# Performance work log

Measured on AMD Instinct MI355X. Metric: run time of the kernel, lower is better.

## Reference

```python
import jax, jax.numpy as jnp
import numpy as np

B, S, D = 4, 2048, 1024


def setup_inputs() -> dict:
    key = jax.random.key(0)
    ks = jax.random.split(key, 7)
    s = 1.0 / np.sqrt(D)
    return {
        "x": jax.random.normal(ks[0], (B, S, D), dtype=jnp.float32),
        "Wq": jax.random.normal(ks[1], (D, D), dtype=jnp.float32) * s,
        "bq": jnp.zeros((D,), dtype=jnp.float32),
        "Wk": jax.random.normal(ks[2], (D, D), dtype=jnp.float32) * s,
        "bk": jnp.zeros((D,), dtype=jnp.float32),
        "Wv": jax.random.normal(ks[3], (D, D), dtype=jnp.float32) * s,
        "bv": jnp.zeros((D,), dtype=jnp.float32),
    }


def reference(x, Wq, bq, Wk, bk, Wv, bv):
    # Linear layers: x @ W^T + b (torch nn.Linear convention)
    Q = jnp.einsum("bsd,ed->bse", x, Wq) + bq
    K = jnp.einsum("bsd,ed->bse", x, Wk) + bk
    V = jnp.einsum("bsd,ed->bse", x, Wv) + bv
    scale = 1.0 / (x.shape[-1] ** 0.5)
    scores = jnp.einsum("bse,bte->bst", Q, K) * scale  # [B, S, S]
    attn = jax.nn.softmax(scores, axis=-1)
    out = jnp.einsum("bst,bte->bse", attn, V)
    return out
```

## Files before the change

### kernel.cpp

```cpp
#include <hip/hip_runtime.h>
#include <math.h>


typedef _Float16 f16;
typedef _Float16 f16x8 __attribute__((ext_vector_type(8)));
typedef _Float16 f16x4 __attribute__((ext_vector_type(4)));
typedef float f32x4 __attribute__((ext_vector_type(4)));

__device__ __forceinline__ void glds16(const void* g, const void* l) {
    __builtin_amdgcn_global_load_lds(
        (const __attribute__((address_space(1))) void*)g,
        (__attribute__((address_space(3))) void*)l, 16, 0, 0);
}

#define VMCNT(n)  asm volatile("s_waitcnt vmcnt(" #n ")" ::: "memory")
#define LGKM(n)   asm volatile("s_waitcnt lgkmcnt(" #n ")" ::: "memory")
#define BARRIER() asm volatile("s_barrier" ::: "memory")
#define SCHEDB()  __builtin_amdgcn_sched_barrier(0)

__global__ __launch_bounds__(256) void cvt16_kernel(
    const float* __restrict__ in, f16* __restrict__ o, int n4)
{
    int i = blockIdx.x * 256 + threadIdx.x;
    if (i >= n4) return;
    float4 v = ((const float4*)in)[i];
    f16x4 h = { (f16)v.x, (f16)v.y, (f16)v.z, (f16)v.w };
    ((f16x4*)o)[i] = h;
}

__global__ __launch_bounds__(256) void cvtw_kernel(
    const float* __restrict__ Wq, const float* __restrict__ Wk,
    const float* __restrict__ Wv, f16* __restrict__ o, int n4)
{
    int i = blockIdx.x * 256 + threadIdx.x;
    if (i >= n4) return;
    const float* src = (blockIdx.y == 0) ? Wq : (blockIdx.y == 1) ? Wk : Wv;
    float4 v = ((const float4*)src)[i];
    f16x4 h = { (f16)v.x, (f16)v.y, (f16)v.z, (f16)v.w };
    ((f16x4*)(o + (size_t)blockIdx.y * 1024 * 1024))[i] = h;
}

__global__ __launch_bounds__(256) void zero_kernel(float* __restrict__ p, int n)
{
    int i = blockIdx.x * 256 + threadIdx.x;
    if (i < n) p[i] = 0.0f;
}

#define ABUF 16384
#define BBUF 8192
#define BOFF 49152

__device__ __forceinline__ void frag_read16(
    const f16* __restrict__ sA, const f16* __restrict__ sB,
    int wr, int wc, int lr, int kq, f16x8 a[2][4], f16x8 b[2][4])
{
    #pragma unroll
    for (int kk = 0; kk < 2; ++kk) {
        const int c = kk * 4 + kq;
        #pragma unroll
        for (int i = 0; i < 4; ++i) {
            const int ar = wr * 64 + i * 16 + lr;
            a[kk][i] = *(const f16x8*)&sA[ar * 64 + ((c ^ (ar & 7)) * 8)];
        }
        #pragma unroll
        for (int j = 0; j < 4; ++j) {
            const int br = wc * 64 + j * 16 + lr;
            b[kk][j] = *(const f16x8*)&sB[br * 64 + ((c ^ (br & 7)) * 8)];
        }
    }
}

__device__ __forceinline__ void mfma32(
    const f16x8 a[2][4], const f16x8 b[2][4], f32x4 acc[4][4])
{
    #pragma unroll
    for (int kk = 0; kk < 2; ++kk)
        #pragma unroll
        for (int i = 0; i < 4; ++i)
            #pragma unroll
            for (int j = 0; j < 4; ++j)
                acc[i][j] = __builtin_amdgcn_mfma_f32_16x16x32_f16(a[kk][i], b[kk][j], acc[i][j], 0, 0, 0);
}

__device__ __forceinline__ void mfma_core3(
    const f16* __restrict__ A, int lda,
    const f16* __restrict__ B, int ldb,
    int K, int m0, int n0, f16* sm, f32x4 acc[4][4])
{
    const int tid  = threadIdx.x;
    const int lane = tid & 63;
    const int w    = tid >> 6;
    const int wr   = w >> 1;
    const int wc   = w & 1;
    const int lr   = lane & 15;
    const int kq   = lane >> 4;

    const int rl = lane >> 3;
    const int ch = (lane & 7) ^ rl;

    const f16* gA[4];
    #pragma unroll
    for (int p = 0; p < 4; ++p)
        gA[p] = A + (size_t)(m0 + p * 64 + w * 8 + rl) * lda + ch * 8;
    const f16* gB[2];
    #pragma unroll
    for (int p = 0; p < 2; ++p)
        gB[p] = B + (size_t)(n0 + p * 64 + w * 8 + rl) * ldb + ch * 8;

    const int NT = K >> 6;

    f16* sA0 = sm;             f16* sB0 = sm + BOFF;
    f16* sA1 = sm + ABUF;      f16* sB1 = sm + BOFF + BBUF;
    f16* sA2 = sm + 2 * ABUF;  f16* sB2 = sm + BOFF + 2 * BBUF;

    #define STAGE(kofs, dA, dB) do {                                          \
        _Pragma("unroll")                                                     \
        for (int p = 0; p < 4; ++p)                                           \
            glds16(gA[p] + (kofs), (dA) + w * 512 + p * 4096);                \
        _Pragma("unroll")                                                     \
        for (int p = 0; p < 2; ++p)                                           \
            glds16(gB[p] + (kofs), (dB) + w * 512 + p * 4096);                \
    } while (0)

    STAGE(0,  sA0, sB0);
    STAGE(64, sA1, sB1);
    VMCNT(6);
    BARRIER();
    f16x8 a0[2][4], b0[2][4], a1[2][4], b1[2][4];
    frag_read16(sA0, sB0, wr, wc, lr, kq, a0, b0);

    for (int t = 0; t < NT; t += 2) {
        if (t + 2 < NT) { STAGE((t + 2) * 64, sA2, sB2); VMCNT(6); }
        else            { VMCNT(0); }
        BARRIER();
        frag_read16(sA1, sB1, wr, wc, lr, kq, a1, b1);
        LGKM(15);
        SCHEDB();
        __builtin_amdgcn_s_setprio(1);
        mfma32(a0, b0, acc);
        __builtin_amdgcn_s_setprio(0);
        BARRIER();

        if (t + 3 < NT) { STAGE((t + 3) * 64, sA0, sB0); }
        if (t + 2 < NT) {
            if (t + 3 < NT) { VMCNT(6); } else { VMCNT(0); }
        }
        BARRIER();
        if (t + 2 < NT) {
            frag_read16(sA2, sB2, wr, wc, lr, kq, a0, b0);
            LGKM(15);
        } else {
            LGKM(0);
        }
        SCHEDB();
        __builtin_amdgcn_s_setprio(1);
        mfma32(a1, b1, acc);
        __builtin_amdgcn_s_setprio(0);
        BARRIER();

        f16* tA = sA2; sA2 = sA1; sA1 = sA0; sA0 = tA;
        f16* tB = sB2; sB2 = sB1; sB1 = sB0; sB0 = tB;
    }
    #undef STAGE
}

__global__ __launch_bounds__(512, 2) void qkv_mfma_kernel(
    const f16* __restrict__ xh, const f16* __restrict__ Wh,
    const float* __restrict__ bq, const float* __restrict__ bk,
    const float* __restrict__ bv,
    f16* __restrict__ Qh, f16* __restrict__ Kh, f16* __restrict__ Vh)
{
    extern __shared__ __align__(16) f16 smem[];
    int flat = blockIdx.x + 8 * (blockIdx.y + 32 * blockIdx.z);
    flat = (flat & 7) * 96 + (flat >> 3);
    const int bx = flat & 7;
    const int by = (flat >> 3) & 31;
    const int bz = flat >> 8;

    const int m0 = by * 256;
    const int n0 = bx * 128;

    f32x4 acc[4][4];
    #pragma unroll
    for (int i = 0; i < 4; ++i)
        #pragma unroll
        for (int j = 0; j < 4; ++j) acc[i][j] = (f32x4){0.f, 0.f, 0.f, 0.f};

    mfma_core3(xh, 1024, Wh + (size_t)bz * 1024 * 1024, 1024, 1024, m0, n0, smem, acc);

    const float* bias = (bz == 0) ? bq : (bz == 1) ? bk : bv;
    const float  sc   = (bz == 0) ? 0.03125f : 1.0f;
    f16* C = (bz == 0) ? Qh : (bz == 1) ? Kh : Vh;
    const int lane = threadIdx.x & 63;
    const int w    = threadIdx.x >> 6;
    const int wr = w >> 1, wc = w & 1;
    const int col  = lane & 15;
    const int quad = lane >> 4;

    #pragma unroll
    for (int j = 0; j < 4; ++j) {
        const int gn = n0 + wc * 64 + j * 16 + col;
        const float bb = bias[gn];
        #pragma unroll
        for (int i = 0; i < 4; ++i)
            #pragma unroll
            for (int r = 0; r < 4; ++r) {
                const int gm = m0 + wr * 64 + i * 16 + quad * 4 + r;
                C[(size_t)gm * 1024 + gn] = (f16)((acc[i][j][r] + bb) * sc);
            }
    }
}

__global__ __launch_bounds__(256) void vtrans_kernel(
    const f16* __restrict__ V, f16* __restrict__ Vt)
{
    __shared__ f16 t[64][72];
    const int b  = blockIdx.z;
    const int s0 = blockIdx.x * 64;
    const int d0 = blockIdx.y * 64;
    const int tid = threadIdx.x;

    const int r  = tid >> 3;
    const int c8 = (tid & 7) * 8;
    const f16* src = V + ((size_t)b * 2048 + s0) * 1024 + d0;
    *(f16x8*)&t[r][c8]      = *(const f16x8*)(src + (size_t)r * 1024 + c8);
    *(f16x8*)&t[r + 32][c8] = *(const f16x8*)(src + (size_t)(r + 32) * 1024 + c8);
    __syncthreads();

    const int dl  = tid >> 2;
    const int sl0 = (tid & 3) * 16;
    f16* dst = Vt + ((size_t)b * 1024 + d0 + dl) * 2048 + s0 + sl0;
    f16 buf[16];
    #pragma unroll
    for (int u = 0; u < 16; ++u) buf[u] = t[sl0 + u][dl];
    *(f16x8*)dst       = *(f16x8*)&buf[0];
    *(f16x8*)(dst + 8) = *(f16x8*)&buf[8];
}

__global__ __launch_bounds__(512, 2) void scores_exp_kernel(
    const f16* __restrict__ Qh, const f16* __restrict__ Kh,
    f16* __restrict__ P, float* __restrict__ sums)
{
    extern __shared__ __align__(16) f16 smem[];
    int flat = blockIdx.x + 16 * (blockIdx.y + 8 * blockIdx.z);
    flat = (flat & 7) * 64 + (flat >> 3);
    const int bx = flat & 15;
    const int by = (flat >> 4) & 7;
    const int b  = flat >> 7;

    const int m0 = by * 256;
    const int n0 = bx * 128;

    f32x4 acc[4][4];
    #pragma unroll
    for (int i = 0; i < 4; ++i)
        #pragma unroll
        for (int j = 0; j < 4; ++j) acc[i][j] = (f32x4){0.f, 0.f, 0.f, 0.f};

    const size_t ao = (size_t)b * 2048 * 1024;
    mfma_core3(Qh + ao, 1024, Kh + ao, 1024, 1024, m0, n0, smem, acc);

    const int lane = threadIdx.x & 63;
    const int w    = threadIdx.x >> 6;
    const int wr = w >> 1, wc = w & 1;
    const int col  = lane & 15;
    const int quad = lane >> 4;
    f16* C = P + (size_t)b * 2048 * 2048;

    float rp[4][4];
    #pragma unroll
    for (int i = 0; i < 4; ++i)
        #pragma unroll
        for (int r = 0; r < 4; ++r) rp[i][r] = 0.0f;

    #pragma unroll
    for (int i = 0; i < 4; ++i)
        #pragma unroll
        for (int r = 0; r < 4; ++r) {
            const int gm = m0 + wr * 64 + i * 16 + quad * 4 + r;
            #pragma unroll
            for (int j = 0; j < 4; ++j) {
                const int gn = n0 + wc * 64 + j * 16 + col;
                const f16 p = (f16)__expf(acc[i][j][r]);
                C[(size_t)gm * 2048 + gn] = p;
                rp[i][r] += (float)p;
            }
        }

    #pragma unroll
    for (int i = 0; i < 4; ++i)
        #pragma unroll
        for (int r = 0; r < 4; ++r) {
            float v = rp[i][r];
            v += __shfl_xor(v, 1);
            v += __shfl_xor(v, 2);
            v += __shfl_xor(v, 4);
            v += __shfl_xor(v, 8);
            rp[i][r] = v;
        }
    if (col == 0) {
        #pragma unroll
        for (int i = 0; i < 4; ++i)
            #pragma unroll
            for (int r = 0; r < 4; ++r) {
                const int row = m0 + wr * 64 + i * 16 + quad * 4 + r;
                atomicAdd(&sums[b * 2048 + row], rp[i][r]);
            }
    }
}

__global__ __launch_bounds__(512, 2) void pv_mfma_kernel(
    const f16* __restrict__ P, const f16* __restrict__ Vt,
    const float* __restrict__ sums, float* __restrict__ out)
{
    extern __shared__ __align__(16) f16 smem[];
    int flat = blockIdx.x + 8 * (blockIdx.y + 8 * blockIdx.z);
    flat = (flat & 7) * 32 + (flat >> 3);
    const int bx = flat & 7;
    const int by = (flat >> 3) & 7;
    const int b  = flat >> 6;

    const int m0 = by * 256;
    const int n0 = bx * 128;

    f32x4 acc[4][4];
    #pragma unroll
    for (int i = 0; i < 4; ++i)
        #pragma unroll
        for (int j = 0; j < 4; ++j) acc[i][j] = (f32x4){0.f, 0.f, 0.f, 0.f};

    const size_t ao = (size_t)b * 2048 * 2048;
    const size_t bo = (size_t)b * 1024 * 2048;
    mfma_core3(P + ao, 2048, Vt + bo, 2048, 2048, m0, n0, smem, acc);

    const int lane = threadIdx.x & 63;
    const int w    = threadIdx.x >> 6;
    const int wr = w >> 1, wc = w & 1;
    const int col  = lane & 15;
    const int quad = lane >> 4;
    float* C = out + (size_t)b * 2048 * 1024;

    #pragma unroll
    for (int i = 0; i < 4; ++i)
        #pragma unroll
        for (int r = 0; r < 4; ++r) {
            const int rowg = m0 + wr * 64 + i * 16 + quad * 4 + r;
            const float inv = 1.0f / sums[b * 2048 + rowg];
            #pragma unroll
            for (int j = 0; j < 4; ++j) {
                const int gn = n0 + wc * 64 + j * 16 + col;
                C[(size_t)rowg * 1024 + gn] = acc[i][j][r] * inv;
            }
        }
}

extern "C" void kernel_launch(void* const* d_in, const int* in_sizes, int n_in,
                              void* d_out, int out_size, void* d_ws, size_t ws_size,
                              hipStream_t stream)
{
    (void)in_sizes; (void)n_in; (void)out_size; (void)ws_size;
    const int Bn = 4, S = 2048, D = 1024;
    const float* x  = (const float*)d_in[0];
    const float* Wq = (const float*)d_in[1];
    const float* bq = (const float*)d_in[2];
    const float* Wk = (const float*)d_in[3];
    const float* bk = (const float*)d_in[4];
    const float* Wv = (const float*)d_in[5];
    const float* bv = (const float*)d_in[6];
    float* out = (float*)d_out;

    const size_t MB = 1024 * 1024;
    char* w = (char*)d_ws;
    f16*   xh   = (f16*)(w + 0 * MB);
    f16*   Wh3  = (f16*)(w + 16 * MB);
    f16*   Vh   = (f16*)(w + 22 * MB);
    f16*   Qh   = (f16*)(w + 38 * MB);
    f16*   Kh   = (f16*)(w + 54 * MB);
    f16*   Vt   = (f16*)(w + 70 * MB);
    float* sums = (float*)(w + 86 * MB);
    f16*   P    = (f16*)(w + 0 * MB);

    static bool attr_set = false;
    if (!attr_set) {
        (void)hipFuncSetAttribute(reinterpret_cast<const void*>(qkv_mfma_kernel),
                            hipFuncAttributeMaxDynamicSharedMemorySize, 147456);
        (void)hipFuncSetAttribute(reinterpret_cast<const void*>(scores_exp_kernel),
                            hipFuncAttributeMaxDynamicSharedMemorySize, 147456);
        (void)hipFuncSetAttribute(reinterpret_cast<const void*>(pv_mfma_kernel),
                            hipFuncAttributeMaxDynamicSharedMemorySize, 147456);
        attr_set = true;
    }

    cvt16_kernel<<<dim3(Bn * S * D / 4 / 256), 256, 0, stream>>>(x, xh, Bn * S * D / 4);
    cvtw_kernel<<<dim3(D * D / 4 / 256, 3), 256, 0, stream>>>(Wq, Wk, Wv, Wh3, D * D / 4);
    zero_kernel<<<dim3((Bn * S + 255) / 256), 256, 0, stream>>>(sums, Bn * S);

    qkv_mfma_kernel<<<dim3(D / 128, (Bn * S) / 256, 3), 512, 147456, stream>>>(
        xh, Wh3, bq, bk, bv, Qh, Kh, Vh);
    vtrans_kernel<<<dim3(S / 64, D / 64, Bn), 256, 0, stream>>>(Vh, Vt);

    scores_exp_kernel<<<dim3(S / 128, S / 256, Bn), 512, 147456, stream>>>(
        Qh, Kh, P, sums);
    pv_mfma_kernel<<<dim3(D / 128, S / 256, Bn), 512, 147456, stream>>>(
        P, Vt, sums, out);
}
```

Baseline: 267.9 us.

## Switch GEMMs to 256x256 tiles with double-buffered interleaved staging core

New measurement: 266.7 us. About the same (-0.4%).

```diff
diff --git a/kernel.cpp b/kernel.cpp
--- a/kernel.cpp
+++ b/kernel.cpp
@@ -46,122 +46,121 @@
     if (i < n) p[i] = 0.0f;
 }
 
-#define ABUF 16384
-#define BBUF 8192
-#define BOFF 49152
-
-__device__ __forceinline__ void frag_read16(
-    const f16* __restrict__ sA, const f16* __restrict__ sB,
-    int wr, int wc, int lr, int kq, f16x8 a[2][4], f16x8 b[2][4])
-{
-    #pragma unroll
-    for (int kk = 0; kk < 2; ++kk) {
-        const int c = kk * 4 + kq;
-        #pragma unroll
-        for (int i = 0; i < 4; ++i) {
-            const int ar = wr * 64 + i * 16 + lr;
-            a[kk][i] = *(const f16x8*)&sA[ar * 64 + ((c ^ (ar & 7)) * 8)];
-        }
-        #pragma unroll
-        for (int j = 0; j < 4; ++j) {
-            const int br = wc * 64 + j * 16 + lr;
-            b[kk][j] = *(const f16x8*)&sB[br * 64 + ((c ^ (br & 7)) * 8)];
-        }
-    }
-}
-
-__device__ __forceinline__ void mfma32(
-    const f16x8 a[2][4], const f16x8 b[2][4], f32x4 acc[4][4])
-{
-    #pragma unroll
-    for (int kk = 0; kk < 2; ++kk)
-        #pragma unroll
-        for (int i = 0; i < 4; ++i)
-            #pragma unroll
-            for (int j = 0; j < 4; ++j)
-                acc[i][j] = __builtin_amdgcn_mfma_f32_16x16x32_f16(a[kk][i], b[kk][j], acc[i][j], 0, 0, 0);
-}
-
-__device__ __forceinline__ void mfma_core3(
+__device__ __forceinline__ void core8(
     const f16* __restrict__ A, int lda,
     const f16* __restrict__ B, int ldb,
-    int K, int m0, int n0, f16* sm, f32x4 acc[4][4])
+    int K, int m0, int n0, f16* sm, f32x4 (&acc)[8][4])
 {
     const int tid  = threadIdx.x;
     const int lane = tid & 63;
     const int w    = tid >> 6;
-    const int wr   = w >> 1;
-    const int wc   = w & 1;
+    const int wr   = w >> 2;
+    const int wn   = w & 3;
     const int lr   = lane & 15;
     const int kq   = lane >> 4;
 
-    const int rl = lane >> 3;
-    const int ch = (lane & 7) ^ rl;
-
-    const f16* gA[4];
-    #pragma unroll
-    for (int p = 0; p < 4; ++p)
-        gA[p] = A + (size_t)(m0 + p * 64 + w * 8 + rl) * lda + ch * 8;
-    const f16* gB[2];
-    #pragma unroll
-    for (int p = 0; p < 2; ++p)
-        gB[p] = B + (size_t)(n0 + p * 64 + w * 8 + rl) * ldb + ch * 8;
-
-    const int NT = K >> 6;
-
-    f16* sA0 = sm;             f16* sB0 = sm + BOFF;
-    f16* sA1 = sm + ABUF;      f16* sB1 = sm + BOFF + BBUF;
-    f16* sA2 = sm + 2 * ABUF;  f16* sB2 = sm + BOFF + 2 * BBUF;
-
-    #define STAGE(kofs, dA, dB) do {                                          \
+    const int rl   = lane >> 3;
+    const int swz  = ((lane & 7) ^ rl) * 8;
+
+    const f16* baseA = A + (size_t)(m0 + w * 16 + rl) * lda + swz;
+    const f16* baseB = B + (size_t)(n0 + w * 16 + rl) * ldb + swz;
+
+    f16* curA = sm;             f16* curB = sm + 16384;
+    f16* othA = sm + 32768;     f16* othB = sm + 49152;
+
+    const int NT   = K >> 6;
+    const int wofs = w * 1024;
+
+    #define STG_A(dst, h, tt) do {                                            \
+        glds16(baseA + (size_t)((h) * 128 + 0) * lda + (size_t)(tt) * 64,     \
+               (dst) + (h) * 8192 + wofs);                                    \
+        glds16(baseA + (size_t)((h) * 128 + 8) * lda + (size_t)(tt) * 64,     \
+               (dst) + (h) * 8192 + wofs + 512);                              \
+    } while (0)
+    #define STG_B(dst, h, tt) do {                                            \
+        glds16(baseB + (size_t)((h) * 128 + 0) * ldb + (size_t)(tt) * 64,     \
+               (dst) + (h) * 8192 + wofs);                                    \
+        glds16(baseB + (size_t)((h) * 128 + 8) * ldb + (size_t)(tt) * 64,     \
+               (dst) + (h) * 8192 + wofs + 512);                              \
+    } while (0)
+    #define RD_A(dst4, mh, kk) do {                                           \
         _Pragma("unroll")                                                     \
-        for (int p = 0; p < 4; ++p)                                           \
-            glds16(gA[p] + (kofs), (dA) + w * 512 + p * 4096);                \
+        for (int i = 0; i < 4; ++i) {                                         \
+            const int ar = wr * 128 + (mh) * 64 + i * 16 + lr;                \
+            dst4[i] = *(const f16x8*)&curA[ar * 64 +                          \
+                        (((((kk) * 4 + kq)) ^ (ar & 7)) * 8)];                \
+        } } while (0)
+    #define RD_B(dst4, kk) do {                                               \
         _Pragma("unroll")                                                     \
-        for (int p = 0; p < 2; ++p)                                           \
-            glds16(gB[p] + (kofs), (dB) + w * 512 + p * 4096);                \
+        for (int j = 0; j < 4; ++j) {                                         \
+            const int br = wn * 64 + j * 16 + lr;                             \
+            dst4[j] = *(const f16x8*)&curB[br * 64 +                          \
+                        (((((kk) * 4 + kq)) ^ (br & 7)) * 8)];                \
+        } } while (0)
+    #define MFMA16(mh, av, bv) do {                                           \
+        _Pragma("unroll")                                                     \
+        for (int i = 0; i < 4; ++i)                                           \
+            _Pragma("unroll")                                                 \
+            for (int j = 0; j < 4; ++j)                                       \
+                acc[(mh) * 4 + i][j] = __builtin_amdgcn_mfma_f32_16x16x32_f16(\
+                    av[i], bv[j], acc[(mh) * 4 + i][j], 0, 0, 0);             \
     } while (0)
 
-    STAGE(0,  sA0, sB0);
-    STAGE(64, sA1, sB1);
-    VMCNT(6);
+    STG_B(curB, 0, 0); STG_B(curB, 1, 0);
+    STG_A(curA, 0, 0); STG_A(curA, 1, 0);
+    STG_B(othB, 0, 1); STG_B(othB, 1, 1);
+    VMCNT(4);
     BARRIER();
-    f16x8 a0[2][4], b0[2][4], a1[2][4], b1[2][4];
-    frag_read16(sA0, sB0, wr, wc, lr, kq, a0, b0);
-
-    for (int t = 0; t < NT; t += 2) {
-        if (t + 2 < NT) { STAGE((t + 2) * 64, sA2, sB2); VMCNT(6); }
-        else            { VMCNT(0); }
-        BARRIER();
-        frag_read16(sA1, sB1, wr, wc, lr, kq, a1, b1);
-        LGKM(15);
-        SCHEDB();
+
+    f16x8 a0[4], a1[4], b0[4], b1[4];
+
+    for (int t = 0; t < NT; ++t) {
+        const bool s1 = (t + 1 < NT);
+        const bool s2 = (t + 2 < NT);
+
+        RD_A(a0, 0, 0); RD_B(b0, 0);
+        if (s1) STG_A(othA, 0, t + 1);
+        BARRIER(); LGKM(0); SCHEDB();
         __builtin_amdgcn_s_setprio(1);
-        mfma32(a0, b0, acc);
+        MFMA16(0, a0, b0);
         __builtin_amdgcn_s_setprio(0);
         BARRIER();
 
-        if (t + 3 < NT) { STAGE((t + 3) * 64, sA0, sB0); }
-        if (t + 2 < NT) {
-            if (t + 3 < NT) { VMCNT(6); } else { VMCNT(0); }
-        }
-        BARRIER();
-        if (t + 2 < NT) {
-            frag_read16(sA2, sB2, wr, wc, lr, kq, a0, b0);
-            LGKM(15);
-        } else {
-            LGKM(0);
-        }
-        SCHEDB();
+        RD_A(a1, 0, 1); RD_B(b1, 1);
+        if (s1) STG_A(othA, 1, t + 1);
+        BARRIER(); LGKM(0); SCHEDB();
         __builtin_amdgcn_s_setprio(1);
-        mfma32(a1, b1, acc);
+        MFMA16(0, a1, b1);
         __builtin_amdgcn_s_setprio(0);
         BARRIER();
 
-        f16* tA = sA2; sA2 = sA1; sA1 = sA0; sA0 = tA;
-        f16* tB = sB2; sB2 = sB1; sB1 = sB0; sB0 = tB;
+        RD_A(a0, 1, 0);
+        if (s2) STG_B(curB, 0, t + 2);
+        BARRIER(); LGKM(0); SCHEDB();
+        __builtin_amdgcn_s_setprio(1);
+        MFMA16(1, a0, b0);
+        __builtin_amdgcn_s_setprio(0);
+        BARRIER();
+
+        RD_A(a1, 1, 1);
+        if (s2) STG_B(curB, 1, t + 2);
+        if (s2)      { VMCNT(4); }
+        else if (s1) { VMCNT(0); }
+        BARRIER(); LGKM(0); SCHEDB();
+        __builtin_amdgcn_s_setprio(1);
+        MFMA16(1, a1, b1);
+        __builtin_amdgcn_s_setprio(0);
+        BARRIER();
+
+        f16* x;
+        x = curA; curA = othA; othA = x;
+        x = curB; curB = othB; othB = x;
     }
-    #undef STAGE
+    #undef STG_A
+    #undef STG_B
+    #undef RD_A
+    #undef RD_B
+    #undef MFMA16
 }
 
 __global__ __launch_bounds__(512, 2) void qkv_mfma_kernel(
@@ -171,41 +170,41 @@
     f16* __restrict__ Qh, f16* __restrict__ Kh, f16* __restrict__ Vh)
 {
     extern __shared__ __align__(16) f16 smem[];
-    int flat = blockIdx.x + 8 * (blockIdx.y + 32 * blockIdx.z);
-    flat = (flat & 7) * 96 + (flat >> 3);
-    const int bx = flat & 7;
-    const int by = (flat >> 3) & 31;
-    const int bz = flat >> 8;
+    int flat = blockIdx.x + 4 * (blockIdx.y + 32 * blockIdx.z);
+    flat = (flat & 7) * 48 + (flat >> 3);
+    const int bx = flat & 3;
+    const int by = (flat >> 2) & 31;
+    const int bz = flat >> 7;
 
     const int m0 = by * 256;
-    const int n0 = bx * 128;
-
-    f32x4 acc[4][4];
-    #pragma unroll
-    for (int i = 0; i < 4; ++i)
+    const int n0 = bx * 256;
+
+    f32x4 acc[8][4];
+    #pragma unroll
+    for (int i = 0; i < 8; ++i)
         #pragma unroll
         for (int j = 0; j < 4; ++j) acc[i][j] = (f32x4){0.f, 0.f, 0.f, 0.f};
 
-    mfma_core3(xh, 1024, Wh + (size_t)bz * 1024 * 1024, 1024, 1024, m0, n0, smem, acc);
+    core8(xh, 1024, Wh + (size_t)bz * 1024 * 1024, 1024, 1024, m0, n0, smem, acc);
 
     const float* bias = (bz == 0) ? bq : (bz == 1) ? bk : bv;
     const float  sc   = (bz == 0) ? 0.03125f : 1.0f;
     f16* C = (bz == 0) ? Qh : (bz == 1) ? Kh : Vh;
     const int lane = threadIdx.x & 63;
     const int w    = threadIdx.x >> 6;
-    const int wr = w >> 1, wc = w & 1;
+    const int wr = w >> 2, wn = w & 3;
     const int col  = lane & 15;
     const int quad = lane >> 4;
 
     #pragma unroll
     for (int j = 0; j < 4; ++j) {
-        const int gn = n0 + wc * 64 + j * 16 + col;
+        const int gn = n0 + wn * 64 + j * 16 + col;
         const float bb = bias[gn];
         #pragma unroll
-        for (int i = 0; i < 4; ++i)
+        for (int i = 0; i < 8; ++i)
             #pragma unroll
             for (int r = 0; r < 4; ++r) {
-                const int gm = m0 + wr * 64 + i * 16 + quad * 4 + r;
+                const int gm = m0 + wr * 128 + i * 16 + quad * 4 + r;
                 C[(size_t)gm * 1024 + gn] = (f16)((acc[i][j][r] + bb) * sc);
             }
     }
@@ -242,45 +241,45 @@
     f16* __restrict__ P, float* __restrict__ sums)
 {
     extern __shared__ __align__(16) f16 smem[];
-    int flat = blockIdx.x + 16 * (blockIdx.y + 8 * blockIdx.z);
-    flat = (flat & 7) * 64 + (flat >> 3);
-    const int bx = flat & 15;
-    const int by = (flat >> 4) & 7;
-    const int b  = flat >> 7;
+    int flat = blockIdx.x + 8 * (blockIdx.y + 8 * blockIdx.z);
+    flat = (flat & 7) * 32 + (flat >> 3);
+    const int bx = flat & 7;
+    const int by = (flat >> 3) & 7;
+    const int b  = flat >> 6;
 
     const int m0 = by * 256;
-    const int n0 = bx * 128;
-
-    f32x4 acc[4][4];
-    #pragma unroll
-    for (int i = 0; i < 4; ++i)
+    const int n0 = bx * 256;
+
+    f32x4 acc[8][4];
+    #pragma unroll
+    for (int i = 0; i < 8; ++i)
         #pragma unroll
         for (int j = 0; j < 4; ++j) acc[i][j] = (f32x4){0.f, 0.f, 0.f, 0.f};
 
     const size_t ao = (size_t)b * 2048 * 1024;
-    mfma_core3(Qh + ao, 1024, Kh + ao, 1024, 1024, m0, n0, smem, acc);
+    core8(Qh + ao, 1024, Kh + ao, 1024, 1024, m0, n0, smem, acc);
 
     const int lane = threadIdx.x & 63;
     const int w    = threadIdx.x >> 6;
-    const int wr = w >> 1, wc = w & 1;
+    const int wr = w >> 2, wn = w & 3;
     const int col  = lane & 15;
     const int quad = lane >> 4;
     f16* C = P + (size_t)b * 2048 * 2048;
 
-    float rp[4][4];
-    #pragma unroll
-    for (int i = 0; i < 4; ++i)
+    float rp[8][4];
+    #pragma unroll
+    for (int i = 0; i < 8; ++i)
         #pragma unroll
         for (int r = 0; r < 4; ++r) rp[i][r] = 0.0f;
 
     #pragma unroll
-    for (int i = 0; i < 4; ++i)
+    for (int i = 0; i < 8; ++i)
         #pragma unroll
         for (int r = 0; r < 4; ++r) {
-            const int gm = m0 + wr * 64 + i * 16 + quad * 4 + r;
+            const int gm = m0 + wr * 128 + i * 16 + quad * 4 + r;
             #pragma unroll
             for (int j = 0; j < 4; ++j) {
-                const int gn = n0 + wc * 64 + j * 16 + col;
+                const int gn = n0 + wn * 64 + j * 16 + col;
                 const f16 p = (f16)__expf(acc[i][j][r]);
                 C[(size_t)gm * 2048 + gn] = p;
                 rp[i][r] += (float)p;
@@ -288,7 +287,7 @@
         }
 
     #pragma unroll
-    for (int i = 0; i < 4; ++i)
+    for (int i = 0; i < 8; ++i)
         #pragma unroll
         for (int r = 0; r < 4; ++r) {
             float v = rp[i][r];
@@ -300,10 +299,10 @@
         }
     if (col == 0) {
         #pragma unroll
-        for (int i = 0; i < 4; ++i)
+        for (int i = 0; i < 8; ++i)
             #pragma unroll
             for (int r = 0; r < 4; ++r) {
-                const int row = m0 + wr * 64 + i * 16 + quad * 4 + r;
+                const int row = m0 + wr * 128 + i * 16 + quad * 4 + r;
                 atomicAdd(&sums[b * 2048 + row], rp[i][r]);
             }
     }
@@ -314,41 +313,41 @@
     const float* __restrict__ sums, float* __restrict__ out)
 {
     extern __shared__ __align__(16) f16 smem[];
-    int flat = blockIdx.x + 8 * (blockIdx.y + 8 * blockIdx.z);
-    flat = (flat & 7) * 32 + (flat >> 3);
-    const int bx = flat & 7;
-    const int by = (flat >> 3) & 7;
-    const int b  = flat >> 6;
+    int flat = blockIdx.x + 4 * (blockIdx.y + 8 * blockIdx.z);
+    flat = (flat & 7) * 16 + (flat >> 3);
+    const int bx = flat & 3;
+    const int by = (flat >> 2) & 7;
+    const int b  = flat >> 5;
 
     const int m0 = by * 256;
-    const int n0 = bx * 128;
-
-    f32x4 acc[4][4];
-    #pragma unroll
-    for (int i = 0; i < 4; ++i)
+    const int n0 = bx * 256;
+
+    f32x4 acc[8][4];
+    #pragma unroll
+    for (int i = 0; i < 8; ++i)
         #pragma unroll
         for (int j = 0; j < 4; ++j) acc[i][j] = (f32x4){0.f, 0.f, 0.f, 0.f};
 
     const size_t ao = (size_t)b * 2048 * 2048;
     const size_t bo = (size_t)b * 1024 * 2048;
-    mfma_core3(P + ao, 2048, Vt + bo, 2048, 2048, m0, n0, smem, acc);
+    core8(P + ao, 2048, Vt + bo, 2048, 2048, m0, n0, smem, acc);
 
     const int lane = threadIdx.x & 63;
     const int w    = threadIdx.x >> 6;
-    const int wr = w >> 1, wc = w & 1;
+    const int wr = w >> 2, wn = w & 3;
     const int col  = lane & 15;
     const int quad = lane >> 4;
     float* C = out + (size_t)b * 2048 * 1024;
 
     #pragma unroll
-    for (int i = 0; i < 4; ++i)
+    for (int i = 0; i < 8; ++i)
         #pragma unroll
         for (int r = 0; r < 4; ++r) {
-            const int rowg = m0 + wr * 64 + i * 16 + quad * 4 + r;
+            const int rowg = m0 + wr * 128 + i * 16 + quad * 4 + r;
             const float inv = 1.0f / sums[b * 2048 + rowg];
             #pragma unroll
             for (int j = 0; j < 4; ++j) {
-                const int gn = n0 + wc * 64 + j * 16 + col;
+                const int gn = n0 + wn * 64 + j * 16 + col;
                 C[(size_t)rowg * 1024 + gn] = acc[i][j][r] * inv;
             }
         }
@@ -383,11 +382,11 @@
     static bool attr_set = false;
     if (!attr_set) {
         (void)hipFuncSetAttribute(reinterpret_cast<const void*>(qkv_mfma_kernel),
-                            hipFuncAttributeMaxDynamicSharedMemorySize, 147456);
+                            hipFuncAttributeMaxDynamicSharedMemorySize, 131072);
         (void)hipFuncSetAttribute(reinterpret_cast<const void*>(scores_exp_kernel),
-                            hipFuncAttributeMaxDynamicSharedMemorySize, 147456);
+                            hipFuncAttributeMaxDynamicSharedMemorySize, 131072);
         (void)hipFuncSetAttribute(reinterpret_cast<const void*>(pv_mfma_kernel),
-                            hipFuncAttributeMaxDynamicSharedMemorySize, 147456);
+                            hipFuncAttributeMaxDynamicSharedMemorySize, 131072);
         attr_set = true;
     }
 
@@ -395,12 +394,12 @@
     cvtw_kernel<<<dim3(D * D / 4 / 256, 3), 256, 0, stream>>>(Wq, Wk, Wv, Wh3, D * D / 4);
     zero_kernel<<<dim3((Bn * S + 255) / 256), 256, 0, stream>>>(sums, Bn * S);
 
-    qkv_mfma_kernel<<<dim3(D / 128, (Bn * S) / 256, 3), 512, 147456, stream>>>(
+    qkv_mfma_kernel<<<dim3(D / 256, (Bn * S) / 256, 3), 512, 131072, stream>>>(
         xh, Wh3, bq, bk, bv, Qh, Kh, Vh);
     vtrans_kernel<<<dim3(S / 64, D / 64, Bn), 256, 0, stream>>>(Vh, Vt);
 
-    scores_exp_kernel<<<dim3(S / 128, S / 256, Bn), 512, 147456, stream>>>(
+    scores_exp_kernel<<<dim3(S / 256, S / 256, Bn), 512, 131072, stream>>>(
         Qh, Kh, P, sums);
-    pv_mfma_kernel<<<dim3(D / 128, S / 256, Bn), 512, 147456, stream>>>(
+    pv_mfma_kernel<<<dim3(D / 256, S / 256, Bn), 512, 131072, stream>>>(
         P, Vt, sums, out);
 }
```
